# Kernel optimization log

Hardware: AMD Instinct MI355X
Metric: run time of the kernel (lower is better)

## Reference

```python
import jax, jax.numpy as jnp
import numpy as np

B = 16384          # batch
N_SPARSE = 16      # single-id sparse features
N_VARLEN = 4       # variable-length sparse features
L = 50             # max sequence length per varlen feature
V = 1_000_000      # vocab per table
D = 1              # linear embedding dim (DeepCTR Linear uses dim=1)
INIT_STD = 1e-4
EPS = 1e-8


def setup_inputs() -> dict:
    key = jax.random.key(0)
    k1, k2, k3 = jax.random.split(key, 3)
    X = jax.random.randint(k1, (B, N_SPARSE + N_VARLEN * L), 0, V, dtype=jnp.int32)
    sparse_tables = jax.random.normal(k2, (N_SPARSE, V, D), dtype=jnp.float32) * INIT_STD
    varlen_tables = jax.random.normal(k3, (N_VARLEN, V, D), dtype=jnp.float32) * INIT_STD
    return {"X": X, "sparse_tables": sparse_tables, "varlen_tables": varlen_tables}


def reference(X, sparse_tables, varlen_tables):
    # --- single-id sparse lookups: one gather per table, vectorized over tables ---
    sparse_ids = X[:, :N_SPARSE]                                  # [B, Ns]
    f_idx = jnp.arange(N_SPARSE)[None, :]                          # [1, Ns]
    sparse_emb = sparse_tables[f_idx, sparse_ids]                  # [B, Ns, D]

    # --- varlen lookups + masked mean pooling (mask: id != 0, DeepCTR convention) ---
    varlen_ids = X[:, N_SPARSE:].reshape(B, N_VARLEN, L)           # [B, Nv, L]
    v_idx = jnp.arange(N_VARLEN)[None, :, None]                    # [1, Nv, 1]
    varlen_emb = varlen_tables[v_idx, varlen_ids]                  # [B, Nv, L, D]
    mask = (varlen_ids != 0).astype(varlen_emb.dtype)[..., None]   # [B, Nv, L, 1]
    summed = jnp.sum(varlen_emb * mask, axis=2)                    # [B, Nv, D]
    lengths = jnp.sum(mask, axis=2)                                # [B, Nv, 1]
    pooled = summed / (lengths + EPS)                              # [B, Nv, D]

    # --- concat and flatten, matching torch.flatten(concat_fun(...), start_dim=1) ---
    out = jnp.concatenate([sparse_emb, pooled], axis=1)            # [B, Ns+Nv, D]
    return out.reshape(B, -1)                                      # [B, (Ns+Nv)*D]
```

## Files before the change

### kernel.cpp

```cpp
#include <hip/hip_runtime.h>

#define B 16384
#define N_SPARSE 16
#define N_VARLEN 4
#define L 50
#define V 1000000
#define ROW (N_SPARSE + N_VARLEN * L)
#define OUT_W (N_SPARSE + N_VARLEN)
#define KLANES 8

__global__ __launch_bounds__(256) void emb_gather_pool_kernel(
    const int* __restrict__ X,
    const float* __restrict__ sparse_tables,
    const float* __restrict__ varlen_tables,
    float* __restrict__ out)
{
    const int tid = blockIdx.x * blockDim.x + threadIdx.x;
    const int SPARSE_THREADS = B * N_SPARSE;

    if (tid < SPARSE_THREADS) {
        const int b = tid >> 4;
        const int j = tid & 15;
        const int id = X[b * ROW + j];
        out[b * OUT_W + j] = sparse_tables[(long)j * V + id];
    } else {
        const int t    = tid - SPARSE_THREADS;
        const int lane = t & (KLANES - 1);
        const int task = t >> 3;
        const int f    = task & (N_VARLEN - 1);
        const int b    = task >> 2;

        const int*   ids = X + b * ROW + N_SPARSE + f * L;
        const float* tab = varlen_tables + (long)f * V;

        float sum = 0.0f;
        float cnt = 0.0f;
        #pragma unroll
        for (int l = lane; l < L; l += KLANES) {
            const int id = ids[l];
            const float v = tab[id];
            const float m = (id != 0) ? 1.0f : 0.0f;
            sum = fmaf(m, v, sum);
            cnt += m;
        }

        #pragma unroll
        for (int off = 1; off < KLANES; off <<= 1) {
            sum += __shfl_xor(sum, off);
            cnt += __shfl_xor(cnt, off);
        }

        if (lane == 0) {
            out[b * OUT_W + N_SPARSE + f] = sum / (cnt + 1e-8f);
        }
    }
}

extern "C" void kernel_launch(void* const* d_in, const int* in_sizes, int n_in,
                              void* d_out, int out_size, void* d_ws, size_t ws_size,
                              hipStream_t stream) {
    const int*   X             = (const int*)  d_in[0];
    const float* sparse_tables = (const float*)d_in[1];
    const float* varlen_tables = (const float*)d_in[2];
    float*       out           = (float*)d_out;

    const int total_threads = B * N_SPARSE + B * N_VARLEN * KLANES;
    const int block = 256;
    const int grid  = (total_threads + block - 1) / block;

    emb_gather_pool_kernel<<<grid, block, 0, stream>>>(X, sparse_tables, varlen_tables, out);
}
```

Measured before the change: 148.9 us.

## Partition varlen blocks by XCD per table and use nontemporal loads/stores

Reorders the grid so varlen blocks come first, and the low bits of the block index (assumed to map to the XCD under round-robin dispatch) pick the table and batch half. Each XCD then gathers from a single varlen table, which is meant to improve L2 locality for table lookups. Id reads, sparse-table reads and output writes switch to nontemporal loads and stores so streaming data does not evict table lines. The benefit depends on the block-to-XCD mapping holding, and the sparse path now runs after the varlen blocks.

Result: faster. 129.5 us (-13.0%).

```diff
diff --git a/kernel.cpp b/kernel.cpp
--- a/kernel.cpp
+++ b/kernel.cpp
@@ -9,35 +9,35 @@
 #define OUT_W (N_SPARSE + N_VARLEN)
 #define KLANES 8
 
+#define VARLEN_BLOCKS 2048
+#define SPARSE_BLOCKS 1024
+
 __global__ __launch_bounds__(256) void emb_gather_pool_kernel(
     const int* __restrict__ X,
     const float* __restrict__ sparse_tables,
     const float* __restrict__ varlen_tables,
     float* __restrict__ out)
 {
-    const int tid = blockIdx.x * blockDim.x + threadIdx.x;
-    const int SPARSE_THREADS = B * N_SPARSE;
+    const int bid = blockIdx.x;
+    const int t   = threadIdx.x;
 
-    if (tid < SPARSE_THREADS) {
-        const int b = tid >> 4;
-        const int j = tid & 15;
-        const int id = X[b * ROW + j];
-        out[b * OUT_W + j] = sparse_tables[(long)j * V + id];
-    } else {
-        const int t    = tid - SPARSE_THREADS;
+    if (bid < VARLEN_BLOCKS) {
+        const int xcd  = bid & 7;
+        const int f    = xcd & 3;
+        const int half = xcd >> 2;
+        const int slot = bid >> 3;
+        const int task = t >> 3;
         const int lane = t & (KLANES - 1);
-        const int task = t >> 3;
-        const int f    = task & (N_VARLEN - 1);
-        const int b    = task >> 2;
+        const int row  = half * (B / 2) + slot * 32 + task;
 
-        const int*   ids = X + b * ROW + N_SPARSE + f * L;
+        const int*   ids = X + row * ROW + N_SPARSE + f * L;
         const float* tab = varlen_tables + (long)f * V;
 
         float sum = 0.0f;
         float cnt = 0.0f;
         #pragma unroll
         for (int l = lane; l < L; l += KLANES) {
-            const int id = ids[l];
+            const int id = __builtin_nontemporal_load(ids + l);
             const float v = tab[id];
             const float m = (id != 0) ? 1.0f : 0.0f;
             sum = fmaf(m, v, sum);
@@ -51,8 +51,18 @@
         }
 
         if (lane == 0) {
-            out[b * OUT_W + N_SPARSE + f] = sum / (cnt + 1e-8f);
+            __builtin_nontemporal_store(sum / (cnt + 1e-8f),
+                                        out + row * OUT_W + N_SPARSE + f);
         }
+    } else {
+        const int sb  = bid - VARLEN_BLOCKS;
+        const int rl  = t >> 4;
+        const int j   = t & 15;
+        const int row = sb * 16 + rl;
+
+        const int   id = __builtin_nontemporal_load(X + row * ROW + j);
+        const float v  = __builtin_nontemporal_load(sparse_tables + (long)j * V + id);
+        __builtin_nontemporal_store(v, out + row * OUT_W + j);
     }
 }
 
@@ -64,9 +74,8 @@
     const float* varlen_tables = (const float*)d_in[2];
     float*       out           = (float*)d_out;
 
-    const int total_threads = B * N_SPARSE + B * N_VARLEN * KLANES;
+    const int grid  = VARLEN_BLOCKS + SPARSE_BLOCKS;
     const int block = 256;
-    const int grid  = (total_threads + block - 1) / block;
 
     emb_gather_pool_kernel<<<grid, block, 0, stream>>>(X, sparse_tables, varlen_tables, out);
 }
```
